# Kernel tuning notes

Measured on AMD Instinct MI355X. Metric: run time of the kernel, lower is better.

Reference implementation:

```python
import jax, jax.numpy as jnp
import numpy as np

HIDDEN = 1024
RANK = 4
N_TASKS = 5
LORA_SCALING = 1.0 / RANK  # lora_alpha / lora_rank = 1/4
LN_EPS = 1e-5


def setup_inputs() -> dict:
    key = jax.random.key(0)
    ks = jax.random.split(key, 9)
    B, S, D = 16, 2048, HIDDEN
    hidden_states = jax.random.normal(ks[0], (B, S, D), dtype=jnp.float32)
    input_tensor = jax.random.normal(ks[1], (B, S, D), dtype=jnp.float32)
    adapter_mask = jax.random.randint(ks[2], (B,), 0, N_TASKS, dtype=jnp.int32)
    W = jax.random.normal(ks[3], (D, D), dtype=jnp.float32) * 0.02
    b = jax.random.normal(ks[4], (D,), dtype=jnp.float32) * 0.02
    lora_A = jax.random.normal(ks[5], (N_TASKS, RANK, D), dtype=jnp.float32) * 0.02
    lora_B = jax.random.normal(ks[6], (N_TASKS, D, RANK), dtype=jnp.float32) * 0.02
    gamma = jnp.ones((D,), dtype=jnp.float32)
    beta = jnp.zeros((D,), dtype=jnp.float32)
    return {
        "hidden_states": hidden_states,
        "input_tensor": input_tensor,
        "W": W,
        "b": b,
        "lora_A": lora_A,
        "lora_B": lora_B,
        "gamma": gamma,
        "beta": beta,
        "adapter_mask": adapter_mask,
    }


def _layernorm(x, gamma, beta):
    mu = jnp.mean(x, axis=-1, keepdims=True)
    xc = x - mu
    var = jnp.mean(xc * xc, axis=-1, keepdims=True)
    return xc * jax.lax.rsqrt(var + LN_EPS) * gamma + beta


def reference(hidden_states, input_tensor, W, b, lora_A, lora_B, gamma, beta, adapter_mask):
    # Base dense projection (first self.dense call)
    h1 = jnp.einsum("bsd,ed->bse", hidden_states, W) + b  # [B,S,D]
    # Per-task LoRA-parametrized dense applied to the projected states
    # (the source loops over unique tasks with gather/scatter; vectorized here
    #  by gathering each batch row's adapter).
    base2 = jnp.einsum("bsd,ed->bse", h1, W) + b  # [B,S,D]
    A_b = lora_A[adapter_mask]  # [B, r, D]
    B_b = lora_B[adapter_mask]  # [B, D, r]
    low = jnp.einsum("bsd,brd->bsr", h1, A_b)  # [B,S,r]
    delta = jnp.einsum("bsr,bdr->bsd", low, B_b)  # [B,S,D]
    h2 = base2 + LORA_SCALING * delta
    # dropout is identity in eval / p=0; residual + LayerNorm
    return _layernorm(h2 + input_tensor, gamma, beta)
```

## Files before the change

### kernel.cpp

```cpp
#include <hip/hip_runtime.h>
#include <hip/hip_bf16.h>
#include <stdint.h>

#define D_HID 1024
#define M_TOT 32768
#define LN_EPS 1e-5f

typedef __bf16 bf16x8 __attribute__((ext_vector_type(8)));
typedef float f32x4 __attribute__((ext_vector_type(4)));
typedef unsigned short u16;
typedef u16 u16x8 __attribute__((ext_vector_type(8)));
typedef u16 u16x4v __attribute__((ext_vector_type(4)));

__device__ __forceinline__ float bf2f(u16 x) {
  union { unsigned int u; float f; } c; c.u = ((unsigned int)x) << 16; return c.f;
}
__device__ __forceinline__ u16 f2bf(float f) {
  union { __bf16 h; u16 u; } c; c.h = (__bf16)f; return c.u;
}
__device__ __forceinline__ void gld16(const u16* g, u16* lds_wave_base) {
  __builtin_amdgcn_global_load_lds(
      (__attribute__((address_space(1))) unsigned int*)g,
      (__attribute__((address_space(3))) unsigned int*)lds_wave_base, 16, 0, 0);
}

__device__ __forceinline__ void cvt_job(const float* __restrict__ hs,
                                        u16* __restrict__ hs_bf, size_t idx) {
  const float4 a = *(const float4*)(hs + idx * 8);
  const float4 b = *(const float4*)(hs + idx * 8 + 4);
  u16x8 o;
  o[0] = f2bf(a.x); o[1] = f2bf(a.y); o[2] = f2bf(a.z); o[3] = f2bf(a.w);
  o[4] = f2bf(b.x); o[5] = f2bf(b.y); o[6] = f2bf(b.z); o[7] = f2bf(b.w);
  *(u16x8*)(hs_bf + idx * 8) = o;
}

#define CVT_K1_BLKS 5440
#define CVT_K2_BLKS 5472
#define CVT_K3_BLKS 5472
#define CVT_K2_OFF  (CVT_K1_BLKS * 256)
#define CVT_K3_OFF  ((CVT_K1_BLKS + CVT_K2_BLKS) * 256)

__global__ __launch_bounds__(256) void k1_prep(
    const float* __restrict__ hs, u16* __restrict__ hs_bf,
    const float* __restrict__ W, u16* __restrict__ hi, u16* __restrict__ lo,
    u16* __restrict__ hiT, u16* __restrict__ loT,
    const float* __restrict__ lA, u16* __restrict__ lAh, u16* __restrict__ lAl) {
  __shared__ float tile[32][33];
  const int bid = blockIdx.x, tid = threadIdx.x;
  if (bid >= 1032) {
    cvt_job(hs, hs_bf, (size_t)(bid - 1032) * 256 + tid);
    return;
  }
  if (bid >= 1024) {
    const int b = bid - 1024;
    for (int i = tid; i < 16 * 1024; i += 256) {
      const int r = b * 16 + (i >> 10), c = i & 1023;
      const float v = (r < 20) ? lA[(size_t)r * 1024 + c] : 0.f;
      const u16 h = f2bf(v);
      lAh[(size_t)r * 1024 + c] = h;
      lAl[(size_t)r * 1024 + c] = f2bf(v - bf2f(h));
    }
    return;
  }
  const int bj = bid & 31, bi = bid >> 5;
  const int tx = tid & 31, ty = tid >> 5;
#pragma unroll
  for (int r0 = 0; r0 < 32; r0 += 8) {
    const int r = r0 + ty;
    const size_t o = (size_t)(bi * 32 + r) * D_HID + bj * 32 + tx;
    const float v = W[o];
    tile[r][tx] = v;
    const u16 h = f2bf(v);
    hi[o] = h; lo[o] = f2bf(v - bf2f(h));
  }
  __syncthreads();
#pragma unroll
  for (int r0 = 0; r0 < 32; r0 += 8) {
    const int r = r0 + ty;
    const float v = tile[tx][r];
    const size_t o = (size_t)(bj * 32 + r) * D_HID + bi * 32 + tx;
    const u16 h = f2bf(v);
    hiT[o] = h; loT[o] = f2bf(v - bf2f(h));
  }
}

__global__ __launch_bounds__(256) void k2_s2(
    const u16* __restrict__ Ah, const u16* __restrict__ Al,
    const u16* __restrict__ Bh, const u16* __restrict__ Bl,
    const u16* __restrict__ lAh, const u16* __restrict__ lAl,
    const float* __restrict__ hs, u16* __restrict__ hs_bf,
    float* __restrict__ C, float* __restrict__ A2) {
  __shared__ __align__(16) u16 smem[4][64 * 32];
  const int bid = blockIdx.x, tid = threadIdx.x;
  if (bid >= 272) {
    cvt_job(hs, hs_bf, (size_t)CVT_K2_OFF + (size_t)(bid - 272) * 256 + tid);
    return;
  }
  const int wave = tid >> 6, lane = tid & 63;
  const int by = bid >> 4, bx = bid & 15;
  const bool isA2 = (by == 16);
  const u16* Asel_h = isA2 ? lAh : Ah;
  const u16* Asel_l = isA2 ? lAl : Al;
  const int arow0 = isA2 ? 0 : by * 64;
  const u16* gsel = (wave == 0) ? Asel_h : (wave == 1) ? Asel_l
                  : (wave == 2) ? Bh : Bl;
  const int rb = (wave < 2) ? arow0 : bx * 64;
  const u16* gp = gsel + (size_t)(rb + (lane >> 2)) * D_HID + (lane & 3) * 8;
  u16* sb = &smem[wave][0];

  const int l15 = lane & 15, quad = lane >> 4;
  const int wm = wave >> 1, wn = wave & 1;
  const int fA = (wm * 32 + l15) * 32 + quad * 8;
  const int fB = (wn * 32 + l15) * 32 + quad * 8;
  f32x4 acc[2][2];
#pragma unroll
  for (int m = 0; m < 2; ++m)
#pragma unroll
    for (int n = 0; n < 2; ++n) acc[m][n] = (f32x4){0.f, 0.f, 0.f, 0.f};

  for (int k0 = 0; k0 < D_HID; k0 += 32) {
    __syncthreads();
#pragma unroll
    for (int q = 0; q < 4; ++q)
      gld16(gp + (size_t)q * 16 * D_HID, sb + q * 512);
    gp += 32;
    __syncthreads();
    bf16x8 ahf[2], alf[2], bhf[2], blf[2];
#pragma unroll
    for (int m = 0; m < 2; ++m) {
      ahf[m] = *(const bf16x8*)(&smem[0][fA + m * 512]);
      alf[m] = *(const bf16x8*)(&smem[1][fA + m * 512]);
    }
#pragma unroll
    for (int n = 0; n < 2; ++n) {
      bhf[n] = *(const bf16x8*)(&smem[2][fB + n * 512]);
      blf[n] = *(const bf16x8*)(&smem[3][fB + n * 512]);
    }
#pragma unroll
    for (int m = 0; m < 2; ++m)
#pragma unroll
      for (int n = 0; n < 2; ++n) {
        acc[m][n] = __builtin_amdgcn_mfma_f32_16x16x32_bf16(ahf[m], bhf[n], acc[m][n], 0, 0, 0);
        acc[m][n] = __builtin_amdgcn_mfma_f32_16x16x32_bf16(alf[m], bhf[n], acc[m][n], 0, 0, 0);
        acc[m][n] = __builtin_amdgcn_mfma_f32_16x16x32_bf16(ahf[m], blf[n], acc[m][n], 0, 0, 0);
      }
  }
  const int nn0 = bx * 64 + wn * 32;
#pragma unroll
  for (int m = 0; m < 2; ++m)
#pragma unroll
    for (int n = 0; n < 2; ++n) {
      const int nn = nn0 + n * 16 + l15;
#pragma unroll
      for (int r = 0; r < 4; ++r) {
        const int lr = wm * 32 + m * 16 + quad * 4 + r;
        if (!isA2) {
          C[(size_t)(by * 64 + lr) * D_HID + nn] = acc[m][n][r];
        } else if (lr < 20) {
          A2[(size_t)lr * D_HID + nn] = acc[m][n][r];
        }
      }
    }
}

__global__ __launch_bounds__(256) void k3_weff(
    const float* __restrict__ Wc, const float* __restrict__ A2,
    const float* __restrict__ lB, const float* __restrict__ lA,
    const float* __restrict__ W, const float* __restrict__ bvec,
    const float* __restrict__ hs, u16* __restrict__ hs_bf,
    u16* __restrict__ Weff, float* __restrict__ beff) {
  const int bid = blockIdx.x, tid = threadIdx.x;
  if (bid >= 5120) {
    cvt_job(hs, hs_bf, (size_t)CVT_K3_OFF + (size_t)(bid - 5120) * 256 + tid);
    return;
  }
  const int n = bid & 1023, t = bid >> 10;
  const int wave = tid >> 6, lane = tid & 63;
  float br[4];
#pragma unroll
  for (int r = 0; r < 4; ++r) br[r] = lB[(size_t)t * 4096 + n * 4 + r];
  float4 v = *(const float4*)(Wc + (size_t)n * D_HID + tid * 4);
#pragma unroll
  for (int r = 0; r < 4; ++r) {
    const float4 a2 = *(const float4*)(A2 + (size_t)(t * 4 + r) * D_HID + tid * 4);
    const float s = 0.25f * br[r];
    v.x += s * a2.x; v.y += s * a2.y; v.z += s * a2.z; v.w += s * a2.w;
  }
  u16x4v o; o[0] = f2bf(v.x); o[1] = f2bf(v.y); o[2] = f2bf(v.z); o[3] = f2bf(v.w);
  *(u16x4v*)(Weff + (size_t)t * 1048576 + (size_t)n * D_HID + tid * 4) = o;
  const float4 bb = *(const float4*)(bvec + tid * 4);
  float p[5];
  {
    const float4 wr = *(const float4*)(W + (size_t)n * D_HID + tid * 4);
    p[0] = wr.x * bb.x + wr.y * bb.y + wr.z * bb.z + wr.w * bb.w;
  }
#pragma unroll
  for (int r = 0; r < 4; ++r) {
    const float4 ar = *(const float4*)(lA + (size_t)(t * 4 + r) * D_HID + tid * 4);
    p[1 + r] = ar.x * bb.x + ar.y * bb.y + ar.z * bb.z + ar.w * bb.w;
  }
#pragma unroll
  for (int m = 1; m < 64; m <<= 1)
#pragma unroll
    for (int jj = 0; jj < 5; ++jj) p[jj] += __shfl_xor(p[jj], m);
  __shared__ float red[4][5];
  if (lane == 0)
#pragma unroll
    for (int jj = 0; jj < 5; ++jj) red[wave][jj] = p[jj];
  __syncthreads();
  if (tid == 0) {
    float P = 0.f, Cr[4] = {0.f, 0.f, 0.f, 0.f};
#pragma unroll
    for (int w = 0; w < 4; ++w) {
      P += red[w][0];
#pragma unroll
      for (int r = 0; r < 4; ++r) Cr[r] += red[w][1 + r];
    }
    const float e = br[0]*Cr[0] + br[1]*Cr[1] + br[2]*Cr[2] + br[3]*Cr[3];
    beff[t * D_HID + n] = P + bvec[n] + 0.25f * e;
  }
}

__global__ __launch_bounds__(512, 1) void gemm_main(
    const u16* __restrict__ Ag, const u16* __restrict__ Wf,
    const float* __restrict__ beff, const int* __restrict__ mask,
    u16* __restrict__ outb) {
  __shared__ __align__(16) u16 sAf[2 * 16384];
  __shared__ __align__(16) u16 sBf[2 * 16384];
  const int tid = threadIdx.x, wave = tid >> 6, lane = tid & 63;
  const int L = blockIdx.x;
  const int xcd = L & 7, j = L >> 3;
  const int bx = j & 3;
  const int by = xcd * 16 + (j >> 2);
  const int task = mask[by >> 3];
  const u16* Bg = Wf + (size_t)task * (D_HID * D_HID);

  const int acol = ((lane & 7) ^ (lane >> 3)) * 8;
  const int aBase = (by * 256 + wave * 8 + (lane >> 3)) * D_HID + acol;
  const int bBase = (bx * 256 + wave * 8 + (lane >> 3)) * D_HID + acol;

  auto stageA = [&](int ktar, int half) {
#pragma unroll
    for (int q = 0; q < 2; ++q)
      gld16(Ag + (aBase + ktar * 64 + half * 131072 + q * 65536),
            sAf + ((ktar & 1) * 16384 + half * 8192 + q * 4096 + wave * 512));
  };
  auto stageB = [&](int ktar, int half) {
#pragma unroll
    for (int q = 0; q < 2; ++q)
      gld16(Bg + (bBase + ktar * 64 + half * 131072 + q * 65536),
            sBf + ((ktar & 1) * 16384 + half * 8192 + q * 4096 + wave * 512));
  };

  const int wm = wave >> 2, wn = wave & 3;
  const int l15 = lane & 15, quad = lane >> 4, l7 = lane & 7;
  const int vA0 = (wm * 128 + l15) * 64 + ((quad ^ l7) * 8);
  const int vB0 = (wn * 64 + l15) * 64 + ((quad ^ l7) * 8);

  f32x4 acc[8][4];
#pragma unroll
  for (int i = 0; i < 8; ++i)
#pragma unroll
    for (int jn = 0; jn < 4; ++jn) acc[i][jn] = (f32x4){0.f, 0.f, 0.f, 0.f};

  stageB(0, 0); stageB(0, 1); stageA(0, 0); stageA(0, 1);
  stageB(1, 0); stageB(1, 1); stageA(1, 0); stageA(1, 1);
  asm volatile("s_waitcnt vmcnt(8)" ::: "memory");
  __builtin_amdgcn_s_barrier();
  __builtin_amdgcn_sched_barrier(0);

  bf16x8 a[4][2], b[4][2];
#pragma unroll 1
  for (int k2 = 0; k2 < 8; ++k2) {
#pragma unroll
    for (int par = 0; par < 2; ++par) {
      const int kt = k2 * 2 + par;
      const u16* pA = sAf + par * 16384;
      const u16* pB = sBf + par * 16384;
      const bool st = (k2 < 7);

#pragma unroll
      for (int m4 = 0; m4 < 4; ++m4) {
        a[m4][0] = *(const bf16x8*)(pA + (vA0 + m4 * 1024));
        a[m4][1] = *(const bf16x8*)(pA + ((vA0 ^ 32) + m4 * 1024));
      }
#pragma unroll
      for (int n2 = 0; n2 < 2; ++n2) {
        b[n2][0] = *(const bf16x8*)(pB + (vB0 + n2 * 1024));
        b[n2][1] = *(const bf16x8*)(pB + ((vB0 ^ 32) + n2 * 1024));
      }
      asm volatile("s_waitcnt lgkmcnt(0)" ::: "memory");
      __builtin_amdgcn_sched_barrier(0);
      __builtin_amdgcn_s_setprio(1);
#pragma unroll
      for (int m4 = 0; m4 < 4; ++m4)
#pragma unroll
        for (int n2 = 0; n2 < 2; ++n2)
#pragma unroll
          for (int kk = 0; kk < 2; ++kk)
            acc[m4][n2] = __builtin_amdgcn_mfma_f32_16x16x32_bf16(
                a[m4][kk], b[n2][kk], acc[m4][n2], 0, 0, 0);
      __builtin_amdgcn_s_setprio(0);

#pragma unroll
      for (int n2 = 0; n2 < 2; ++n2) {
        b[2 + n2][0] = *(const bf16x8*)(pB + (vB0 + (2 + n2) * 1024));
        b[2 + n2][1] = *(const bf16x8*)(pB + ((vB0 ^ 32) + (2 + n2) * 1024));
      }
      asm volatile("s_waitcnt lgkmcnt(0)" ::: "memory");
      __builtin_amdgcn_sched_barrier(0);
      __builtin_amdgcn_s_setprio(1);
#pragma unroll
      for (int m4 = 0; m4 < 4; ++m4)
#pragma unroll
        for (int n2 = 0; n2 < 2; ++n2)
#pragma unroll
          for (int kk = 0; kk < 2; ++kk)
            acc[m4][2 + n2] = __builtin_amdgcn_mfma_f32_16x16x32_bf16(
                a[m4][kk], b[2 + n2][kk], acc[m4][2 + n2], 0, 0, 0);
      __builtin_amdgcn_s_setprio(0);
      __builtin_amdgcn_s_barrier();
      __builtin_amdgcn_sched_barrier(0);

#pragma unroll
      for (int m4 = 0; m4 < 4; ++m4) {
        a[m4][0] = *(const bf16x8*)(pA + (vA0 + (4 + m4) * 1024));
        a[m4][1] = *(const bf16x8*)(pA + ((vA0 ^ 32) + (4 + m4) * 1024));
      }
      if (st) { stageB(kt + 2, 0); stageB(kt + 2, 1); }
      asm volatile("s_waitcnt lgkmcnt(0)" ::: "memory");
      __builtin_amdgcn_sched_barrier(0);
      __builtin_amdgcn_s_setprio(1);
#pragma unroll
      for (int m4 = 0; m4 < 4; ++m4)
#pragma unroll
        for (int n2 = 0; n2 < 2; ++n2)
#pragma unroll
          for (int kk = 0; kk < 2; ++kk)
            acc[4 + m4][n2] = __builtin_amdgcn_mfma_f32_16x16x32_bf16(
                a[m4][kk], b[n2][kk], acc[4 + m4][n2], 0, 0, 0);
      __builtin_amdgcn_s_setprio(0);
      __builtin_amdgcn_s_barrier();
      __builtin_amdgcn_sched_barrier(0);

      if (st) { stageA(kt + 2, 0); stageA(kt + 2, 1); }
      __builtin_amdgcn_s_setprio(1);
#pragma unroll
      for (int m4 = 0; m4 < 4; ++m4)
#pragma unroll
        for (int n2 = 0; n2 < 2; ++n2)
#pragma unroll
          for (int kk = 0; kk < 2; ++kk)
            acc[4 + m4][2 + n2] = __builtin_amdgcn_mfma_f32_16x16x32_bf16(
                a[m4][kk], b[2 + n2][kk], acc[4 + m4][2 + n2], 0, 0, 0);
      __builtin_amdgcn_s_setprio(0);
      if (st)            { asm volatile("s_waitcnt vmcnt(8)" ::: "memory"); }
      else if (par == 0) { asm volatile("s_waitcnt vmcnt(0)" ::: "memory"); }
      __builtin_amdgcn_s_barrier();
      __builtin_amdgcn_sched_barrier(0);
    }
  }

  const float* bb = beff + task * D_HID;
  const size_t mBase = (size_t)by * 256 + wm * 128;
  const int nb0 = bx * 256 + wn * 64;
#pragma unroll
  for (int mf = 0; mf < 8; ++mf)
#pragma unroll
    for (int nf = 0; nf < 4; ++nf) {
      const int n = nb0 + nf * 16 + l15;
      const float bval = bb[n];
#pragma unroll
      for (int r = 0; r < 4; ++r) {
        const size_t m = mBase + mf * 16 + quad * 4 + r;
        outb[m * 2048 + n] = f2bf(acc[mf][nf][r] + bval);
      }
    }
}

__global__ __launch_bounds__(256) void ln4(float* __restrict__ out,
                                           const float* __restrict__ resid,
                                           const float* __restrict__ gamma,
                                           const float* __restrict__ beta) {
  const int row = blockIdx.x * 4 + (threadIdx.x >> 6);
  const int lane = threadIdx.x & 63;
  const u16* hb = (const u16*)out + (size_t)row * 2048;
  const float* rp = resid + (size_t)row * D_HID;
  float* po = out + (size_t)row * D_HID;
  float4 v[4];
#pragma unroll
  for (int k = 0; k < 4; ++k) {
    const int c = lane * 4 + k * 256;
    const u16x4v h = *(const u16x4v*)(hb + c);
    const float4 r = *(const float4*)(rp + c);
    v[k].x = bf2f(h[0]) + r.x; v[k].y = bf2f(h[1]) + r.y;
    v[k].z = bf2f(h[2]) + r.z; v[k].w = bf2f(h[3]) + r.w;
  }
  float s = 0.f, q = 0.f;
#pragma unroll
  for (int k = 0; k < 4; ++k) {
    s += v[k].x + v[k].y + v[k].z + v[k].w;
    q += v[k].x * v[k].x + v[k].y * v[k].y + v[k].z * v[k].z + v[k].w * v[k].w;
  }
#pragma unroll
  for (int m = 1; m < 64; m <<= 1) { s += __shfl_xor(s, m); q += __shfl_xor(q, m); }
  const float mu  = s * (1.f / (float)D_HID);
  const float var = q * (1.f / (float)D_HID) - mu * mu;
  const float inv = rsqrtf(var + LN_EPS);
#pragma unroll
  for (int k = 0; k < 4; ++k) {
    const int c = lane * 4 + k * 256;
    const float4 g  = *(const float4*)(gamma + c);
    const float4 bb = *(const float4*)(beta + c);
    float4 o;
    o.x = (v[k].x - mu) * inv * g.x + bb.x;
    o.y = (v[k].y - mu) * inv * g.y + bb.y;
    o.z = (v[k].z - mu) * inv * g.z + bb.z;
    o.w = (v[k].w - mu) * inv * g.w + bb.w;
    *(float4*)(po + c) = o;
  }
}

extern "C" void kernel_launch(void* const* d_in, const int* in_sizes, int n_in,
                              void* d_out, int out_size, void* d_ws, size_t ws_size,
                              hipStream_t stream) {
  const float* hs    = (const float*)d_in[0];
  const float* inp   = (const float*)d_in[1];
  const float* W     = (const float*)d_in[2];
  const float* b     = (const float*)d_in[3];
  const float* lA    = (const float*)d_in[4];
  const float* lB    = (const float*)d_in[5];
  const float* gamma = (const float*)d_in[6];
  const float* beta  = (const float*)d_in[7];
  const int*   mask  = (const int*)d_in[8];
  float* out = (float*)d_out;

  char* wsb = (char*)d_ws;
  u16*   hs_bf = (u16*)wsb;
  float* Wc    = (float*)(wsb + 67108864);
  u16*   weff  = (u16*)(wsb + 71303168);
  u16*   Whi   = weff;
  u16*   Wlo   = weff + 1048576;
  u16*   WhiT  = weff + 2097152;
  u16*   WloT  = weff + 3145728;
  u16*   lAh   = weff + 4194304;
  u16*   lAl   = weff + 4325376;
  float* A2    = (float*)(wsb + 81788928);
  float* beff  = (float*)(wsb + 81871360);

  k1_prep<<<1032 + CVT_K1_BLKS, 256, 0, stream>>>(
      hs, hs_bf, W, Whi, Wlo, WhiT, WloT, lA, lAh, lAl);
  k2_s2<<<272 + CVT_K2_BLKS, 256, 0, stream>>>(
      Whi, Wlo, WhiT, WloT, lAh, lAl, hs, hs_bf, Wc, A2);
  k3_weff<<<5120 + CVT_K3_BLKS, 256, 0, stream>>>(
      Wc, A2, lB, lA, W, b, hs, hs_bf, weff, beff);
  gemm_main<<<512, 512, 0, stream>>>(hs_bf, weff, beff, mask, (u16*)out);
  ln4<<<M_TOT / 4, 256, 0, stream>>>(out, inp, gamma, beta);
}
```

Baseline: 457.9 us.

## Halve GEMM K-tile to 32 and shrink LDS to allow multiple blocks per CU

Reduces the main GEMM K-step from 64 to 32, halving the LDS double buffers and restructuring the pipeline to two MFMA phases per step with a single global-load issue point. Launch bounds now request 4 blocks per CU so several workgroups can co-reside and hide latency. The trade is twice as many barriers and K iterations, and the register budget at 4 blocks of 512 threads may force spills of the 128-float accumulator.

```diff
diff --git a/kernel.cpp b/kernel.cpp
--- a/kernel.cpp
+++ b/kernel.cpp
@@ -221,12 +221,12 @@
   }
 }
 
-__global__ __launch_bounds__(512, 1) void gemm_main(
+__global__ __launch_bounds__(512, 4) void gemm_main(
     const u16* __restrict__ Ag, const u16* __restrict__ Wf,
     const float* __restrict__ beff, const int* __restrict__ mask,
     u16* __restrict__ outb) {
-  __shared__ __align__(16) u16 sAf[2 * 16384];
-  __shared__ __align__(16) u16 sBf[2 * 16384];
+  __shared__ __align__(16) u16 sAf[2 * 8192];
+  __shared__ __align__(16) u16 sBf[2 * 8192];
   const int tid = threadIdx.x, wave = tid >> 6, lane = tid & 63;
   const int L = blockIdx.x;
   const int xcd = L & 7, j = L >> 3;
@@ -235,27 +235,24 @@
   const int task = mask[by >> 3];
   const u16* Bg = Wf + (size_t)task * (D_HID * D_HID);
 
-  const int acol = ((lane & 7) ^ (lane >> 3)) * 8;
-  const int aBase = (by * 256 + wave * 8 + (lane >> 3)) * D_HID + acol;
-  const int bBase = (bx * 256 + wave * 8 + (lane >> 3)) * D_HID + acol;
-
-  auto stageA = [&](int ktar, int half) {
-#pragma unroll
-    for (int q = 0; q < 2; ++q)
-      gld16(Ag + (aBase + ktar * 64 + half * 131072 + q * 65536),
-            sAf + ((ktar & 1) * 16384 + half * 8192 + q * 4096 + wave * 512));
+  const int so = ((lane & 3) ^ ((lane >> 3) & 3)) * 8;
+  const int arow = wave * 16 + (lane >> 2);
+  const int aB0 = (by * 256 + arow) * D_HID + so;
+  const int bB0 = (bx * 256 + arow) * D_HID + so;
+  auto stageA = [&](int kt, int half) {
+    gld16(Ag + aB0 + half * 128 * D_HID + kt * 32,
+          sAf + (kt & 1) * 8192 + half * 4096 + wave * 512);
   };
-  auto stageB = [&](int ktar, int half) {
-#pragma unroll
-    for (int q = 0; q < 2; ++q)
-      gld16(Bg + (bBase + ktar * 64 + half * 131072 + q * 65536),
-            sBf + ((ktar & 1) * 16384 + half * 8192 + q * 4096 + wave * 512));
+  auto stageB = [&](int kt, int half) {
+    gld16(Bg + bB0 + half * 128 * D_HID + kt * 32,
+          sBf + (kt & 1) * 8192 + half * 4096 + wave * 512);
   };
 
   const int wm = wave >> 2, wn = wave & 3;
-  const int l15 = lane & 15, quad = lane >> 4, l7 = lane & 7;
-  const int vA0 = (wm * 128 + l15) * 64 + ((quad ^ l7) * 8);
-  const int vB0 = (wn * 64 + l15) * 64 + ((quad ^ l7) * 8);
+  const int l15 = lane & 15, quad = lane >> 4;
+  const int sw = (l15 >> 1) & 3;
+  const int vA0 = (wm * 128 + l15) * 32 + ((quad ^ sw) * 8);
+  const int vB0 = (wn * 64 + l15) * 32 + ((quad ^ sw) * 8);
 
   f32x4 acc[8][4];
 #pragma unroll
@@ -265,97 +262,54 @@
 
   stageB(0, 0); stageB(0, 1); stageA(0, 0); stageA(0, 1);
   stageB(1, 0); stageB(1, 1); stageA(1, 0); stageA(1, 1);
-  asm volatile("s_waitcnt vmcnt(8)" ::: "memory");
+  asm volatile("s_waitcnt vmcnt(4)" ::: "memory");
   __builtin_amdgcn_s_barrier();
   __builtin_amdgcn_sched_barrier(0);
 
-  bf16x8 a[4][2], b[4][2];
+  bf16x8 a[4], b[4];
 #pragma unroll 1
-  for (int k2 = 0; k2 < 8; ++k2) {
+  for (int k2 = 0; k2 < 16; ++k2) {
 #pragma unroll
     for (int par = 0; par < 2; ++par) {
       const int kt = k2 * 2 + par;
-      const u16* pA = sAf + par * 16384;
-      const u16* pB = sBf + par * 16384;
-      const bool st = (k2 < 7);
-
-#pragma unroll
-      for (int m4 = 0; m4 < 4; ++m4) {
-        a[m4][0] = *(const bf16x8*)(pA + (vA0 + m4 * 1024));
-        a[m4][1] = *(const bf16x8*)(pA + ((vA0 ^ 32) + m4 * 1024));
-      }
-#pragma unroll
-      for (int n2 = 0; n2 < 2; ++n2) {
-        b[n2][0] = *(const bf16x8*)(pB + (vB0 + n2 * 1024));
-        b[n2][1] = *(const bf16x8*)(pB + ((vB0 ^ 32) + n2 * 1024));
-      }
+      const u16* pA = sAf + par * 8192;
+      const u16* pB = sBf + par * 8192;
+      const bool st = (kt < 30);
+
+#pragma unroll
+      for (int nf = 0; nf < 4; ++nf) b[nf] = *(const bf16x8*)(pB + vB0 + nf * 512);
+#pragma unroll
+      for (int mf = 0; mf < 4; ++mf) a[mf] = *(const bf16x8*)(pA + vA0 + mf * 512);
       asm volatile("s_waitcnt lgkmcnt(0)" ::: "memory");
       __builtin_amdgcn_sched_barrier(0);
       __builtin_amdgcn_s_setprio(1);
 #pragma unroll
-      for (int m4 = 0; m4 < 4; ++m4)
-#pragma unroll
-        for (int n2 = 0; n2 < 2; ++n2)
-#pragma unroll
-          for (int kk = 0; kk < 2; ++kk)
-            acc[m4][n2] = __builtin_amdgcn_mfma_f32_16x16x32_bf16(
-                a[m4][kk], b[n2][kk], acc[m4][n2], 0, 0, 0);
+      for (int mf = 0; mf < 4; ++mf)
+#pragma unroll
+        for (int nf = 0; nf < 4; ++nf)
+          acc[mf][nf] = __builtin_amdgcn_mfma_f32_16x16x32_bf16(
+              a[mf], b[nf], acc[mf][nf], 0, 0, 0);
       __builtin_amdgcn_s_setprio(0);
 
 #pragma unroll
-      for (int n2 = 0; n2 < 2; ++n2) {
-        b[2 + n2][0] = *(const bf16x8*)(pB + (vB0 + (2 + n2) * 1024));
-        b[2 + n2][1] = *(const bf16x8*)(pB + ((vB0 ^ 32) + (2 + n2) * 1024));
-      }
+      for (int mf = 0; mf < 4; ++mf)
+        a[mf] = *(const bf16x8*)(pA + vA0 + (4 + mf) * 512);
       asm volatile("s_waitcnt lgkmcnt(0)" ::: "memory");
       __builtin_amdgcn_sched_barrier(0);
-      __builtin_amdgcn_s_setprio(1);
-#pragma unroll
-      for (int m4 = 0; m4 < 4; ++m4)
-#pragma unroll
-        for (int n2 = 0; n2 < 2; ++n2)
-#pragma unroll
-          for (int kk = 0; kk < 2; ++kk)
-            acc[m4][2 + n2] = __builtin_amdgcn_mfma_f32_16x16x32_bf16(
-                a[m4][kk], b[2 + n2][kk], acc[m4][2 + n2], 0, 0, 0);
-      __builtin_amdgcn_s_setprio(0);
       __builtin_amdgcn_s_barrier();
       __builtin_amdgcn_sched_barrier(0);
-
-#pragma unroll
-      for (int m4 = 0; m4 < 4; ++m4) {
-        a[m4][0] = *(const bf16x8*)(pA + (vA0 + (4 + m4) * 1024));
-        a[m4][1] = *(const bf16x8*)(pA + ((vA0 ^ 32) + (4 + m4) * 1024));
-      }
-      if (st) { stageB(kt + 2, 0); stageB(kt + 2, 1); }
-      asm volatile("s_waitcnt lgkmcnt(0)" ::: "memory");
-      __builtin_amdgcn_sched_barrier(0);
+      if (st) { stageB(kt + 2, 0); stageB(kt + 2, 1);
+                stageA(kt + 2, 0); stageA(kt + 2, 1); }
       __builtin_amdgcn_s_setprio(1);
 #pragma unroll
-      for (int m4 = 0; m4 < 4; ++m4)
-#pragma unroll
-        for (int n2 = 0; n2 < 2; ++n2)
-#pragma unroll
-          for (int kk = 0; kk < 2; ++kk)
-            acc[4 + m4][n2] = __builtin_amdgcn_mfma_f32_16x16x32_bf16(
-                a[m4][kk], b[n2][kk], acc[4 + m4][n2], 0, 0, 0);
+      for (int mf = 0; mf < 4; ++mf)
+#pragma unroll
+        for (int nf = 0; nf < 4; ++nf)
+          acc[4 + mf][nf] = __builtin_amdgcn_mfma_f32_16x16x32_bf16(
+              a[mf], b[nf], acc[4 + mf][nf], 0, 0, 0);
       __builtin_amdgcn_s_setprio(0);
-      __builtin_amdgcn_s_barrier();
-      __builtin_amdgcn_sched_barrier(0);
-
-      if (st) { stageA(kt + 2, 0); stageA(kt + 2, 1); }
-      __builtin_amdgcn_s_setprio(1);
-#pragma unroll
-      for (int m4 = 0; m4 < 4; ++m4)
-#pragma unroll
-        for (int n2 = 0; n2 < 2; ++n2)
-#pragma unroll
-          for (int kk = 0; kk < 2; ++kk)
-            acc[4 + m4][2 + n2] = __builtin_amdgcn_mfma_f32_16x16x32_bf16(
-                a[m4][kk], b[2 + n2][kk], acc[4 + m4][2 + n2], 0, 0, 0);
-      __builtin_amdgcn_s_setprio(0);
-      if (st)            { asm volatile("s_waitcnt vmcnt(8)" ::: "memory"); }
-      else if (par == 0) { asm volatile("s_waitcnt vmcnt(0)" ::: "memory"); }
+      if (st)             { asm volatile("s_waitcnt vmcnt(4)" ::: "memory"); }
+      else if (kt == 30)  { asm volatile("s_waitcnt vmcnt(0)" ::: "memory"); }
       __builtin_amdgcn_s_barrier();
       __builtin_amdgcn_sched_barrier(0);
     }
```

Measured after the change: 917.9 us. 100% more time.
